# Kernel tuning notes

Measured on AMD Instinct MI355X. Metric: run time of the kernel, lower is better.

The kernel has to match this reference:

```python
import jax, jax.numpy as jnp
import numpy as np
from jax import lax

MAX_MEMORY_LR = 0.2
MIN_MEMORY_DECAY = 0.5
MEMORY_MAX_NORM = 15.0
NORM_EPS = 1e-6

def _inv_sig(x):
    x = max(min(x, 0.999), 0.001)
    return float(np.log(x / (1 - x)))

def setup_inputs() -> dict:
    key = jax.random.key(0)
    k1, k2 = jax.random.split(key)
    B, S, D = 16, 4096, 256
    x = jax.random.normal(k1, (B, S, D), dtype=jnp.float32)
    # xavier_uniform with gain=0.1 on (d_out, d_in)
    limit = 0.1 * float(np.sqrt(6.0 / (D + D)))
    M_init = jax.random.uniform(k2, (D, D), dtype=jnp.float32, minval=-limit, maxval=limit)
    eta_raw = jnp.asarray(_inv_sig(0.05), dtype=jnp.float32)
    alpha_raw = jnp.asarray(_inv_sig(0.9), dtype=jnp.float32)
    return {"x": x, "M_init": M_init, "eta_raw": eta_raw, "alpha_raw": alpha_raw}

def reference(x, M_init, eta_raw, alpha_raw):
    # x: [B, S, d_in], M_init: [d_out, d_in]
    B = x.shape[0]
    eta = jax.nn.sigmoid(eta_raw) * MAX_MEMORY_LR
    alpha = MIN_MEMORY_DECAY + jax.nn.sigmoid(alpha_raw) * (1.0 - MIN_MEMORY_DECAY)
    M0 = jnp.broadcast_to(M_init, (B,) + M_init.shape)

    def step(M, x_t):  # M: [B, d_out, d_in], x_t: [B, d_in]
        out_t = jnp.einsum('boi,bi->bo', M, x_t)  # retrieve
        # key = F.normalize(x_t): x / max(||x||, eps)
        k = x_t / jnp.maximum(jnp.linalg.norm(x_t, axis=-1, keepdims=True), NORM_EPS)
        Mk = jnp.einsum('boi,bi->bo', M, k)
        err = out_t - Mk  # value is out_t (self-generated)
        M_new = alpha * M + eta * err[:, :, None] * k[:, None, :]  # rank-1 delta update
        fro = jnp.sqrt(jnp.sum(M_new * M_new, axis=(-2, -1), keepdims=True))
        scale = jnp.minimum(MEMORY_MAX_NORM / (fro + 1e-6), 1.0)
        return M_new * scale, out_t

    M_final, outs = lax.scan(step, M0, jnp.swapaxes(x, 0, 1))
    return jnp.swapaxes(outs, 0, 1), M_final
```

## Files before the change

kernel.cpp:

```cpp
#include <hip/hip_runtime.h>
#include <hip/hip_bf16.h>
#include <math.h>

typedef float  f32x4  __attribute__((ext_vector_type(4)));
typedef short  bf16x4 __attribute__((ext_vector_type(4)));
typedef __bf16 bfv4   __attribute__((ext_vector_type(4)));

#define B_    16
#define S_    4096
#define D_    256
#define CK_   16
#define NC_   (S_ / CK_)
#define NP_   (NC_ / 2)
#define PBLOB_ 1664
#define W_    4

__device__ __forceinline__ f32x4 mfma_bf16(bf16x4 a, bf16x4 b, f32x4 c) {
#if defined(__has_builtin) && __has_builtin(__builtin_amdgcn_mfma_f32_16x16x16bf16_1k)
    return __builtin_amdgcn_mfma_f32_16x16x16bf16_1k(a, b, c, 0, 0, 0);
#else
    f32x4 d;
    asm("v_mfma_f32_16x16x16_bf16 %0, %1, %2, %3" : "=v"(d) : "v"(a), "v"(b), "v"(c));
    return d;
#endif
}
__device__ __forceinline__ bf16x4 pk4(f32x4 v) {
    bfv4 h;
    h[0] = (__bf16)v[0]; h[1] = (__bf16)v[1]; h[2] = (__bf16)v[2]; h[3] = (__bf16)v[3];
    return __builtin_bit_cast(bf16x4, h);
}
__device__ __forceinline__ f32x4 up4(bf16x4 h) {
    f32x4 r;
    r[0] = __uint_as_float(((unsigned)(unsigned short)h[0]) << 16);
    r[1] = __uint_as_float(((unsigned)(unsigned short)h[1]) << 16);
    r[2] = __uint_as_float(((unsigned)(unsigned short)h[2]) << 16);
    r[3] = __uint_as_float(((unsigned)(unsigned short)h[3]) << 16);
    return r;
}

__global__ __launch_bounds__(64) void ldm_prep(
    const float* __restrict__ x,
    const float* __restrict__ eta_raw,
    const float* __restrict__ alpha_raw,
    unsigned char* __restrict__ blob)
{
    const int lane = threadIdx.x;
    const int b = blockIdx.x >> 7;
    const int p = blockIdx.x & (NP_ - 1);
    const int l15 = lane & 15;
    const int q   = lane >> 4;

    __shared__ float Ga[256], Gb[256], Gxs[256];
    __shared__ float csh[32];
    __shared__ float Ts[2][256];

    const float* xa = x + ((size_t)b * S_ + (size_t)p * 32 + l15) * D_ + q * 4;
    const float* xc = xa + 16 * D_;

    const f32x4 z = {0,0,0,0};
    f32x4 ga1=z, ga2=z, ga3=z, gb1=z, gb2=z, gb3=z, gx1=z, gx2=z, gx3=z;
    #pragma unroll 4
    for (int kb = 0; kb < 16; ++kb) {
        f32x4 va = *(const f32x4*)(xa + kb * 16);
        f32x4 vb = *(const f32x4*)(xc + kb * 16);
        bf16x4 ha = pk4(va), la = pk4(va - up4(ha));
        bf16x4 hb = pk4(vb), lb = pk4(vb - up4(hb));
        ga1 = mfma_bf16(ha, ha, ga1);
        ga2 = mfma_bf16(ha, la, ga2);
        ga3 = mfma_bf16(la, ha, ga3);
        gb1 = mfma_bf16(hb, hb, gb1);
        gb2 = mfma_bf16(hb, lb, gb2);
        gb3 = mfma_bf16(lb, hb, gb3);
        gx1 = mfma_bf16(hb, ha, gx1);
        gx2 = mfma_bf16(hb, la, gx2);
        gx3 = mfma_bf16(lb, ha, gx3);
    }
    f32x4 ga = (ga1 + ga2) + ga3;
    f32x4 gb = (gb1 + gb2) + gb3;
    f32x4 gx = (gx1 + gx2) + gx3;
    *(f32x4*)(&Ga[l15 * 16 + q * 4]) = ga;
    *(f32x4*)(&Gb[l15 * 16 + q * 4]) = gb;
    #pragma unroll
    for (int r = 0; r < 4; ++r) Gxs[(q * 4 + r) * 16 + l15] = gx[r];
    __syncthreads();

    const float eta   = 0.2f / (1.0f + expf(-eta_raw[0]));
    const float alpha = 0.5f + 0.5f / (1.0f + expf(-alpha_raw[0]));
    if (lane < 32) {
        const float* G = (lane < 16) ? Ga : Gb;
        float gtt = G[l15 * 17];
        float n   = fmaxf(sqrtf(gtt), 1e-6f);
        float inv = 1.0f / n;
        csh[lane] = eta * (1.0f - inv) * inv / alpha;
    }
    __syncthreads();

    if (lane < 32) {
        const int j = l15;
        const float* G  = (lane < 16) ? Ga : Gb;
        const float* cp = (lane < 16) ? csh : csh + 16;
        float cr[16];
        #pragma unroll
        for (int k = 0; k < 16; ++k) cr[k] = cp[k];
        float Tcol[16];
        Tcol[0] = 0.f;
        #pragma unroll
        for (int t = 1; t < 16; ++t) {
            float acc = cr[j] * G[t * 16 + j];
            #pragma unroll
            for (int k = 1; k < 15; ++k)
                if (k < t) acc += cr[k] * G[t * 16 + k] * Tcol[k];
            Tcol[t] = (t > j) ? acc : 0.f;
        }
        float* Tsj = Ts[lane >> 4];
        #pragma unroll
        for (int t = 0; t < 16; ++t) Tsj[t * 16 + j] = Tcol[t];
    }
    __syncthreads();

    unsigned char* bp = blob + (size_t)(b * NP_ + p) * PBLOB_;
    const int idx = l15 * 16 + q * 4;
    *(bf16x4*)(bp + idx * 2)        = pk4(*(const f32x4*)(&Ts[0][idx]));
    *(bf16x4*)(bp + 512 + idx * 2)  = pk4(*(const f32x4*)(&Ts[1][idx]));
    *(bf16x4*)(bp + 1024 + idx * 2) = pk4(*(const f32x4*)(&Gxs[idx]));
    if (lane < 32) ((float*)(bp + 1536))[lane] = csh[lane];
}

__global__ __launch_bounds__(256, 1) void ldm_main(
    const float* __restrict__ x,
    const float* __restrict__ Minit,
    const float* __restrict__ alpha_raw,
    const unsigned char* __restrict__ blob,
    float* __restrict__ out)
{
    const int tid    = threadIdx.x;
    const int lane   = tid & 63;
    const int w      = __builtin_amdgcn_readfirstlane(tid >> 6);
    const int batch  = blockIdx.x >> 4;
    const int rowblk = blockIdx.x & 15;
    const int l15    = lane & 15;
    const int q      = lane >> 4;
    const int col0   = w * 64;

    __shared__ f32x4 parts[2][W_][2][64];

    const float alpha = 0.5f + 0.5f / (1.0f + expf(-alpha_raw[0]));
    const float a2 = alpha * alpha, a4 = a2 * a2, a8 = a4 * a4, a16 = a8 * a8;
    const float a32 = a16 * a16;
    const float aq = (q == 0) ? 1.f : (q == 1) ? a4 : (q == 2) ? a8 : a8 * a4;
    const f32x4 apowA = { aq, aq * alpha, aq * a2, aq * a2 * alpha };
    const f32x4 apowB = apowA * a16;

    const int s = l15 - (q << 2);
    bf16x4 IB;
    IB[0] = (s == 0) ? (short)0x3F80 : (short)0;
    IB[1] = (s == 1) ? (short)0x3F80 : (short)0;
    IB[2] = (s == 2) ? (short)0x3F80 : (short)0;
    IB[3] = (s == 3) ? (short)0x3F80 : (short)0;

    const int mrow = rowblk * 16 + l15;
    f32x4 master[4];
    #pragma unroll
    for (int cb = 0; cb < 4; ++cb)
        master[cb] = *(const f32x4*)(Minit + (size_t)mrow * D_ + col0 + cb * 16 + q * 4);

    const float* xbb = x + (size_t)batch * S_ * D_;
    const unsigned char* bb0 = blob + (size_t)batch * NP_ * PBLOB_;
    const int tfoff = (l15 * 16 + q * 4) * 2;

    const float* xr = xbb + (size_t)l15 * D_ + col0 + q * 4;
    const float* xptr;
    const unsigned char* bptr;
    float* outpj = out + (size_t)batch * S_ * D_ + rowblk * 16 + l15
                 + (size_t)q * 4 * D_;

    struct BlobT { bf16x4 Ta, Tb, Gx; f32x4 ca, cb; };
    BlobT bA, bB;
    bf16x4 XA[8], XB[8];
    f32x4  Xf[8];
    const f32x4 zz = {0,0,0,0};

    {
        #pragma unroll
        for (int cb = 0; cb < 4; ++cb) {
            Xf[cb]     = *(const f32x4*)(xr + cb * 16);
            Xf[4 + cb] = *(const f32x4*)(xr + 16 * D_ + cb * 16);
        }
        #pragma unroll
        for (int i = 0; i < 8; ++i) XA[i] = pk4(Xf[i]);
        bA.Ta = *(const bf16x4*)(bb0 + tfoff);
        bA.Tb = *(const bf16x4*)(bb0 + 512 + tfoff);
        bA.Gx = *(const bf16x4*)(bb0 + 1024 + tfoff);
        bA.ca = *(const f32x4*)(bb0 + 1536 + q * 16);
        bA.cb = *(const f32x4*)(bb0 + 1600 + q * 16);
        xptr = xr + 32 * D_;
        bptr = bb0 + PBLOB_;
    }

    auto body = [&](int j, bf16x4 (&Xc)[8], bf16x4 (&Xn)[8], BlobT& bc, BlobT& bn) {
        const int par = j & 1;
        #pragma unroll
        for (int cb = 0; cb < 4; ++cb) {
            Xf[cb]     = *(const f32x4*)(xptr + cb * 16);
            Xf[4 + cb] = *(const f32x4*)(xptr + 16 * D_ + cb * 16);
        }
        bn.Ta = *(const bf16x4*)(bptr + tfoff);
        bn.Tb = *(const bf16x4*)(bptr + 512 + tfoff);
        bn.Gx = *(const bf16x4*)(bptr + 1024 + tfoff);
        bn.ca = *(const f32x4*)(bptr + 1536 + q * 16);
        bn.cb = *(const f32x4*)(bptr + 1600 + q * 16);
        if (j < NP_ - 2) { xptr += 32 * D_; bptr += PBLOB_; }

        bf16x4 mf[4];
        #pragma unroll
        for (int cb = 0; cb < 4; ++cb) mf[cb] = pk4(master[cb]);
        f32x4 acca = zz, accb = zz;
        #pragma unroll
        for (int cb = 0; cb < 4; ++cb) {
            acca = mfma_bf16(Xc[cb],     mf[cb], acca);
            accb = mfma_bf16(Xc[4 + cb], mf[cb], accb);
        }
        parts[par][w][0][lane] = acca;
        parts[par][w][1][lane] = accb;

        bf16x4 ta[4], tb[4];
        #pragma unroll
        for (int cb = 0; cb < 4; ++cb) {
            ta[cb] = pk4(mfma_bf16(Xc[cb],     IB, zz));
            tb[cb] = pk4(mfma_bf16(Xc[4 + cb], IB, zz));
        }
        __syncthreads();

        f32x4 pa0 = parts[par][0][0][lane], pa1 = parts[par][1][0][lane];
        f32x4 pa2 = parts[par][2][0][lane], pa3 = parts[par][3][0][lane];
        f32x4 pb0 = parts[par][0][1][lane], pb1 = parts[par][1][1][lane];
        f32x4 pb2 = parts[par][2][1][lane], pb3 = parts[par][3][1][lane];
        f32x4 bba = (pa0 + pa1) + (pa2 + pa3);
        f32x4 bbb = (pb0 + pb1) + (pb2 + pb3);

        f32x4 da = mfma_bf16(bc.Ta, pk4(bba), bba);
        if (w == 2) {
            #pragma unroll
            for (int r = 0; r < 4; ++r) outpj[r * D_] = da[r] * apowA[r];
        }
        bf16x4 ea = pk4(da * bc.ca);
        f32x4 bb2 = mfma_bf16(bc.Gx, ea, bbb);
        f32x4 db = mfma_bf16(bc.Tb, pk4(bb2), bb2);
        if (w == 3) {
            #pragma unroll
            for (int r = 0; r < 4; ++r) outpj[(16 + r) * D_] = db[r] * apowB[r];
        }
        bf16x4 eb = pk4(db * bc.cb);

        #pragma unroll
        for (int cb = 0; cb < 4; ++cb) {
            f32x4 m = mfma_bf16(ta[cb], ea, master[cb]);
            master[cb] = mfma_bf16(tb[cb], eb, m) * a32;
        }

        #pragma unroll
        for (int i = 0; i < 8; ++i) Xn[i] = pk4(Xf[i]);
        outpj += 32 * D_;
    };

    for (int j = 0; j < NP_; j += 2) {
        body(j,     XA, XB, bA, bB);
        body(j + 1, XB, XA, bB, bA);
    }

    float* Mout = out + (size_t)B_ * S_ * D_
                + ((size_t)batch * D_ + mrow) * D_;
    #pragma unroll
    for (int cb = 0; cb < 4; ++cb)
        *(f32x4*)(Mout + col0 + cb * 16 + q * 4) = master[cb];
}

extern "C" void kernel_launch(void* const* d_in, const int* in_sizes, int n_in,
                              void* d_out, int out_size, void* d_ws, size_t ws_size,
                              hipStream_t stream) {
    const float* x         = (const float*)d_in[0];
    const float* Minit     = (const float*)d_in[1];
    const float* eta_raw   = (const float*)d_in[2];
    const float* alpha_raw = (const float*)d_in[3];
    float* out = (float*)d_out;
    unsigned char* blob = (unsigned char*)d_ws;

    hipLaunchKernelGGL(ldm_prep, dim3(B_ * NP_), dim3(64), 0, stream,
                       x, eta_raw, alpha_raw, blob);
    hipLaunchKernelGGL(ldm_main, dim3(B_ * 16), dim3(256), 0, stream,
                       x, Minit, alpha_raw, blob, out);
}
```

Before: 280.4 us.

## Solve full 32-step triangular system in prep and software-pipeline main loop

```diff
diff --git a/kernel.cpp b/kernel.cpp
--- a/kernel.cpp
+++ b/kernel.cpp
@@ -50,9 +50,9 @@
     const int l15 = lane & 15;
     const int q   = lane >> 4;
 
-    __shared__ float Ga[256], Gb[256], Gxs[256];
+    __shared__ float G32[1024];
     __shared__ float csh[32];
-    __shared__ float Ts[2][256];
+    __shared__ float Ts32[1024];
 
     const float* xa = x + ((size_t)b * S_ + (size_t)p * 32 + l15) * D_ + q * 4;
     const float* xc = xa + 16 * D_;
@@ -78,17 +78,16 @@
     f32x4 ga = (ga1 + ga2) + ga3;
     f32x4 gb = (gb1 + gb2) + gb3;
     f32x4 gx = (gx1 + gx2) + gx3;
-    *(f32x4*)(&Ga[l15 * 16 + q * 4]) = ga;
-    *(f32x4*)(&Gb[l15 * 16 + q * 4]) = gb;
+    *(f32x4*)(&G32[l15 * 32 + q * 4]) = ga;
+    *(f32x4*)(&G32[(16 + l15) * 32 + 16 + q * 4]) = gb;
     #pragma unroll
-    for (int r = 0; r < 4; ++r) Gxs[(q * 4 + r) * 16 + l15] = gx[r];
+    for (int r = 0; r < 4; ++r) G32[(16 + q * 4 + r) * 32 + l15] = gx[r];
     __syncthreads();
 
     const float eta   = 0.2f / (1.0f + expf(-eta_raw[0]));
     const float alpha = 0.5f + 0.5f / (1.0f + expf(-alpha_raw[0]));
     if (lane < 32) {
-        const float* G = (lane < 16) ? Ga : Gb;
-        float gtt = G[l15 * 17];
+        float gtt = G32[lane * 33];
         float n   = fmaxf(sqrtf(gtt), 1e-6f);
         float inv = 1.0f / n;
         csh[lane] = eta * (1.0f - inv) * inv / alpha;
@@ -96,33 +95,30 @@
     __syncthreads();
 
     if (lane < 32) {
-        const int j = l15;
-        const float* G  = (lane < 16) ? Ga : Gb;
-        const float* cp = (lane < 16) ? csh : csh + 16;
-        float cr[16];
-        #pragma unroll
-        for (int k = 0; k < 16; ++k) cr[k] = cp[k];
-        float Tcol[16];
+        const int j = lane;
+        float cr[32];
+        #pragma unroll
+        for (int k = 0; k < 32; ++k) cr[k] = csh[k];
+        float Tcol[32];
         Tcol[0] = 0.f;
         #pragma unroll
-        for (int t = 1; t < 16; ++t) {
-            float acc = cr[j] * G[t * 16 + j];
+        for (int t = 1; t < 32; ++t) {
+            float acc = cr[j] * G32[t * 32 + j];
             #pragma unroll
-            for (int k = 1; k < 15; ++k)
-                if (k < t) acc += cr[k] * G[t * 16 + k] * Tcol[k];
+            for (int k = 1; k < 31; ++k)
+                if (k < t) acc += cr[k] * G32[t * 32 + k] * Tcol[k];
             Tcol[t] = (t > j) ? acc : 0.f;
         }
-        float* Tsj = Ts[lane >> 4];
-        #pragma unroll
-        for (int t = 0; t < 16; ++t) Tsj[t * 16 + j] = Tcol[t];
+        #pragma unroll
+        for (int t = 0; t < 32; ++t) Ts32[t * 32 + j] = Tcol[t];
     }
     __syncthreads();
 
     unsigned char* bp = blob + (size_t)(b * NP_ + p) * PBLOB_;
     const int idx = l15 * 16 + q * 4;
-    *(bf16x4*)(bp + idx * 2)        = pk4(*(const f32x4*)(&Ts[0][idx]));
-    *(bf16x4*)(bp + 512 + idx * 2)  = pk4(*(const f32x4*)(&Ts[1][idx]));
-    *(bf16x4*)(bp + 1024 + idx * 2) = pk4(*(const f32x4*)(&Gxs[idx]));
+    *(bf16x4*)(bp + idx * 2)        = pk4(*(const f32x4*)(&Ts32[l15 * 32 + q * 4]));
+    *(bf16x4*)(bp + 512 + idx * 2)  = pk4(*(const f32x4*)(&Ts32[(16 + l15) * 32 + 16 + q * 4]));
+    *(bf16x4*)(bp + 1024 + idx * 2) = pk4(*(const f32x4*)(&Ts32[(16 + l15) * 32 + q * 4]));
     if (lane < 32) ((float*)(bp + 1536))[lane] = csh[lane];
 }
 
@@ -169,15 +165,14 @@
     const int tfoff = (l15 * 16 + q * 4) * 2;
 
     const float* xr = xbb + (size_t)l15 * D_ + col0 + q * 4;
-    const float* xptr;
-    const unsigned char* bptr;
     float* outpj = out + (size_t)batch * S_ * D_ + rowblk * 16 + l15
                  + (size_t)q * 4 * D_;
 
-    struct BlobT { bf16x4 Ta, Tb, Gx; f32x4 ca, cb; };
+    struct BlobT { bf16x4 Ta, Tbb, Tba; f32x4 ca, cb; };
     BlobT bA, bB;
-    bf16x4 XA[8], XB[8];
+    bf16x4 Xn[8];
     f32x4  Xf[8];
+    bf16x4 ta[4], tb[4];
     const f32x4 zz = {0,0,0,0};
 
     {
@@ -186,86 +181,107 @@
             Xf[cb]     = *(const f32x4*)(xr + cb * 16);
             Xf[4 + cb] = *(const f32x4*)(xr + 16 * D_ + cb * 16);
         }
-        #pragma unroll
-        for (int i = 0; i < 8; ++i) XA[i] = pk4(Xf[i]);
-        bA.Ta = *(const bf16x4*)(bb0 + tfoff);
-        bA.Tb = *(const bf16x4*)(bb0 + 512 + tfoff);
-        bA.Gx = *(const bf16x4*)(bb0 + 1024 + tfoff);
-        bA.ca = *(const f32x4*)(bb0 + 1536 + q * 16);
-        bA.cb = *(const f32x4*)(bb0 + 1600 + q * 16);
-        xptr = xr + 32 * D_;
-        bptr = bb0 + PBLOB_;
-    }
-
-    auto body = [&](int j, bf16x4 (&Xc)[8], bf16x4 (&Xn)[8], BlobT& bc, BlobT& bn) {
+        bA.Ta  = *(const bf16x4*)(bb0 + tfoff);
+        bA.Tbb = *(const bf16x4*)(bb0 + 512 + tfoff);
+        bA.Tba = *(const bf16x4*)(bb0 + 1024 + tfoff);
+        bA.ca  = *(const f32x4*)(bb0 + 1536 + q * 16);
+        bA.cb  = *(const f32x4*)(bb0 + 1600 + q * 16);
+        const unsigned char* b1 = bb0 + PBLOB_;
+        bB.Ta  = *(const bf16x4*)(b1 + tfoff);
+        bB.Tbb = *(const bf16x4*)(b1 + 512 + tfoff);
+        bB.Tba = *(const bf16x4*)(b1 + 1024 + tfoff);
+        bB.ca  = *(const f32x4*)(b1 + 1536 + q * 16);
+        bB.cb  = *(const f32x4*)(b1 + 1600 + q * 16);
+        #pragma unroll
+        for (int i = 0; i < 8; ++i) Xn[i] = pk4(Xf[i]);
+        const float* x1 = xr + 32 * D_;
+        #pragma unroll
+        for (int cb = 0; cb < 4; ++cb) {
+            Xf[cb]     = *(const f32x4*)(x1 + cb * 16);
+            Xf[4 + cb] = *(const f32x4*)(x1 + 16 * D_ + cb * 16);
+        }
+        bf16x4 mf[4];
+        #pragma unroll
+        for (int cb = 0; cb < 4; ++cb) mf[cb] = pk4(master[cb]);
+        f32x4 acca = mfma_bf16(Xn[1], mf[1], mfma_bf16(Xn[0], mf[0], zz))
+                   + mfma_bf16(Xn[3], mf[3], mfma_bf16(Xn[2], mf[2], zz));
+        f32x4 accb = mfma_bf16(Xn[5], mf[1], mfma_bf16(Xn[4], mf[0], zz))
+                   + mfma_bf16(Xn[7], mf[3], mfma_bf16(Xn[6], mf[2], zz));
+        parts[0][w][0][lane] = acca;
+        parts[0][w][1][lane] = accb;
+        #pragma unroll
+        for (int cb = 0; cb < 4; ++cb) {
+            ta[cb] = pk4(mfma_bf16(Xn[cb],     IB, zz));
+            tb[cb] = pk4(mfma_bf16(Xn[4 + cb], IB, zz));
+        }
+        __syncthreads();
+    }
+
+    const float* xptr = xr + (size_t)2 * 32 * D_;
+    const unsigned char* bptrE = bb0 + 2 * PBLOB_;
+    const unsigned char* bptrO = bb0 + 3 * PBLOB_;
+
+    auto iter = [&](int j, BlobT& bc, const unsigned char*& bptr) {
         const int par = j & 1;
-        #pragma unroll
-        for (int cb = 0; cb < 4; ++cb) {
-            Xf[cb]     = *(const f32x4*)(xptr + cb * 16);
-            Xf[4 + cb] = *(const f32x4*)(xptr + 16 * D_ + cb * 16);
-        }
-        bn.Ta = *(const bf16x4*)(bptr + tfoff);
-        bn.Tb = *(const bf16x4*)(bptr + 512 + tfoff);
-        bn.Gx = *(const bf16x4*)(bptr + 1024 + tfoff);
-        bn.ca = *(const f32x4*)(bptr + 1536 + q * 16);
-        bn.cb = *(const f32x4*)(bptr + 1600 + q * 16);
-        if (j < NP_ - 2) { xptr += 32 * D_; bptr += PBLOB_; }
-
-        bf16x4 mf[4];
-        #pragma unroll
-        for (int cb = 0; cb < 4; ++cb) mf[cb] = pk4(master[cb]);
-        f32x4 acca = zz, accb = zz;
-        #pragma unroll
-        for (int cb = 0; cb < 4; ++cb) {
-            acca = mfma_bf16(Xc[cb],     mf[cb], acca);
-            accb = mfma_bf16(Xc[4 + cb], mf[cb], accb);
-        }
-        parts[par][w][0][lane] = acca;
-        parts[par][w][1][lane] = accb;
-
-        bf16x4 ta[4], tb[4];
-        #pragma unroll
-        for (int cb = 0; cb < 4; ++cb) {
-            ta[cb] = pk4(mfma_bf16(Xc[cb],     IB, zz));
-            tb[cb] = pk4(mfma_bf16(Xc[4 + cb], IB, zz));
-        }
-        __syncthreads();
-
         f32x4 pa0 = parts[par][0][0][lane], pa1 = parts[par][1][0][lane];
         f32x4 pa2 = parts[par][2][0][lane], pa3 = parts[par][3][0][lane];
         f32x4 pb0 = parts[par][0][1][lane], pb1 = parts[par][1][1][lane];
         f32x4 pb2 = parts[par][2][1][lane], pb3 = parts[par][3][1][lane];
+        #pragma unroll
+        for (int i = 0; i < 8; ++i) Xn[i] = pk4(Xf[i]);
+        #pragma unroll
+        for (int cb = 0; cb < 4; ++cb) {
+            Xf[cb]     = *(const f32x4*)(xptr + cb * 16);
+            Xf[4 + cb] = *(const f32x4*)(xptr + 16 * D_ + cb * 16);
+        }
+        if (j < NP_ - 3) xptr += 32 * D_;
         f32x4 bba = (pa0 + pa1) + (pa2 + pa3);
         f32x4 bbb = (pb0 + pb1) + (pb2 + pb3);
-
-        f32x4 da = mfma_bf16(bc.Ta, pk4(bba), bba);
+        bf16x4 baF = pk4(bba), bbF = pk4(bbb);
+        f32x4 da = mfma_bf16(bc.Ta, baF, bba);
+        f32x4 db = mfma_bf16(bc.Tba, baF, mfma_bf16(bc.Tbb, bbF, bbb));
         if (w == 2) {
             #pragma unroll
             for (int r = 0; r < 4; ++r) outpj[r * D_] = da[r] * apowA[r];
         }
-        bf16x4 ea = pk4(da * bc.ca);
-        f32x4 bb2 = mfma_bf16(bc.Gx, ea, bbb);
-        f32x4 db = mfma_bf16(bc.Tb, pk4(bb2), bb2);
         if (w == 3) {
             #pragma unroll
             for (int r = 0; r < 4; ++r) outpj[(16 + r) * D_] = db[r] * apowB[r];
         }
+        bf16x4 ea = pk4(da * bc.ca);
         bf16x4 eb = pk4(db * bc.cb);
-
+        bc.Ta  = *(const bf16x4*)(bptr + tfoff);
+        bc.Tbb = *(const bf16x4*)(bptr + 512 + tfoff);
+        bc.Tba = *(const bf16x4*)(bptr + 1024 + tfoff);
+        bc.ca  = *(const f32x4*)(bptr + 1536 + q * 16);
+        bc.cb  = *(const f32x4*)(bptr + 1600 + q * 16);
+        if (j < NP_ - 4) bptr += 2 * PBLOB_;
         #pragma unroll
         for (int cb = 0; cb < 4; ++cb) {
             f32x4 m = mfma_bf16(ta[cb], ea, master[cb]);
             master[cb] = mfma_bf16(tb[cb], eb, m) * a32;
         }
-
-        #pragma unroll
-        for (int i = 0; i < 8; ++i) Xn[i] = pk4(Xf[i]);
+        bf16x4 mf[4];
+        #pragma unroll
+        for (int cb = 0; cb < 4; ++cb) mf[cb] = pk4(master[cb]);
+        f32x4 acca = mfma_bf16(Xn[1], mf[1], mfma_bf16(Xn[0], mf[0], zz))
+                   + mfma_bf16(Xn[3], mf[3], mfma_bf16(Xn[2], mf[2], zz));
+        f32x4 accb = mfma_bf16(Xn[5], mf[1], mfma_bf16(Xn[4], mf[0], zz))
+                   + mfma_bf16(Xn[7], mf[3], mfma_bf16(Xn[6], mf[2], zz));
+        parts[par ^ 1][w][0][lane] = acca;
+        parts[par ^ 1][w][1][lane] = accb;
+        #pragma unroll
+        for (int cb = 0; cb < 4; ++cb) {
+            ta[cb] = pk4(mfma_bf16(Xn[cb],     IB, zz));
+            tb[cb] = pk4(mfma_bf16(Xn[4 + cb], IB, zz));
+        }
         outpj += 32 * D_;
+        __syncthreads();
     };
 
     for (int j = 0; j < NP_; j += 2) {
-        body(j,     XA, XB, bA, bB);
-        body(j + 1, XB, XA, bB, bA);
+        iter(j,     bA, bptrE);
+        iter(j + 1, bB, bptrO);
     }
 
     float* Mout = out + (size_t)B_ * S_ * D_
```

Result: slower. 321.3 us (+14.5%).
